# Kernel optimization log

Measured on AMD Instinct MI355X. Metric: run time of the kernel, lower is better.

Reference implementation:

```python
import jax, jax.numpy as jnp
import numpy as np

EXP = 1          # module init arg `exp`
NEG = -1e9       # masked_fill value


def setup_inputs() -> dict:
    key = jax.random.key(0)
    k1, k2 = jax.random.split(key)
    lhs = jax.random.normal(k1, (8, 1023, 768), dtype=jnp.float32)
    rhs = jax.random.normal(k2, (8, 8192, 768), dtype=jnp.float32)
    return {"lhs": lhs, "rhs": rhs}


def reference(lhs, rhs):
    # lhs: [B, N_1, dim], rhs: [B, N_, dim], N = N_1 + 1, F = N_ // N
    B, N1, d = lhs.shape
    N = N1 + 1
    Ntot = rhs.shape[1]
    F = Ntot // N

    # L2-normalize along feature dim (normalize_vector)
    ln = lhs / jnp.linalg.norm(lhs, axis=-1, keepdims=True)
    rn = rhs / jnp.linalg.norm(rhs, axis=-1, keepdims=True)

    # cosine similarity: [B, N_1, N_]
    sim = jnp.einsum('bnd,bmd->bnm', ln, rn) ** EXP

    # Diagonal-window mask on the [B, N_1, F, N] view:
    #  - column 0 of each N-block -> NEG
    #  - last N_1 columns (indices 1..N_1) -> NEG except where col-1 == row
    keep = jnp.concatenate(
        [jnp.zeros((N1, 1), dtype=bool), jnp.eye(N1, dtype=bool)], axis=-1
    )  # [N_1, N]
    sim4 = sim.reshape(B, N1, F, N)
    sim4 = jnp.where(keep[None, :, None, :], sim4, NEG)
    return sim4.reshape(B, N1, Ntot)
```

## Files before the change

### kernel.cpp

```cpp
#include <hip/hip_runtime.h>

constexpr int B    = 8;
constexpr int N1   = 1023;
constexpr int NBLK = 1024;
constexpr int D    = 768;
constexpr int F    = 8;
constexpr int NTOT = 8192;
constexpr float NEG = -1e9f;

typedef float v4f __attribute__((ext_vector_type(4)));

__global__ __launch_bounds__(256)
void lcs_kernel(const float* __restrict__ lhs,
                const float* __restrict__ rhs,
                float* __restrict__ out) {
    int t    = threadIdx.x;
    int wave = t >> 6;
    int lane = t & 63;

    int bid = blockIdx.x;
    int g   = bid / 9;
    int p   = bid - g * 9;

    v4f neg4 = {NEG, NEG, NEG, NEG};

    if (p == 0) {
        int row = g * 4 + wave;
        int n   = row % N1;
        int ol  = ((n + 1) >> 2) >> 3;

        v4f* o4 = (v4f*)out + (size_t)row * (NTOT / 4);
        #pragma unroll
        for (int it = 0; it < 32; ++it) {
            if (((it * 8 + (lane >> 3)) & 31) != ol) {
                __builtin_nontemporal_store(neg4, &o4[it * 64 + lane]);
            }
        }
    } else {
        int dot_id = g * 8 + (p - 1);
        int gi     = dot_id * 4 + wave;

        int n   = gi % N1;
        int tmp = gi / N1;
        int f   = tmp % F;
        int b   = tmp / F;

        const v4f* l4 = (const v4f*)(lhs + ((size_t)b * N1 + n) * D);
        const v4f* r4 = (const v4f*)(rhs + ((size_t)b * NTOT + (size_t)f * NBLK + (n + 1)) * D);

        v4f a0 = l4[lane];
        v4f a1 = l4[lane + 64];
        v4f a2 = l4[lane + 128];
        v4f c0 = __builtin_nontemporal_load(&r4[lane]);
        v4f c1 = __builtin_nontemporal_load(&r4[lane + 64]);
        v4f c2 = __builtin_nontemporal_load(&r4[lane + 128]);

        float dot = a0.x*c0.x + a0.y*c0.y + a0.z*c0.z + a0.w*c0.w
                  + a1.x*c1.x + a1.y*c1.y + a1.z*c1.z + a1.w*c1.w
                  + a2.x*c2.x + a2.y*c2.y + a2.z*c2.z + a2.w*c2.w;
        float l2  = a0.x*a0.x + a0.y*a0.y + a0.z*a0.z + a0.w*a0.w
                  + a1.x*a1.x + a1.y*a1.y + a1.z*a1.z + a1.w*a1.w
                  + a2.x*a2.x + a2.y*a2.y + a2.z*a2.z + a2.w*a2.w;
        float r2  = c0.x*c0.x + c0.y*c0.y + c0.z*c0.z + c0.w*c0.w
                  + c1.x*c1.x + c1.y*c1.y + c1.z*c1.z + c1.w*c1.w
                  + c2.x*c2.x + c2.y*c2.y + c2.z*c2.z + c2.w*c2.w;

        #pragma unroll
        for (int off = 32; off >= 1; off >>= 1) {
            dot += __shfl_xor(dot, off, 64);
            l2  += __shfl_xor(l2,  off, 64);
            r2  += __shfl_xor(r2,  off, 64);
        }
        float sim = dot * rsqrtf(l2 * r2);

        int keep_col = n + 1;
        int q_seg    = keep_col >> 2;
        int own_base = q_seg & ~7;
        if (lane < 8) {
            int qidx = own_base + lane;
            v4f v = neg4;
            if (qidx == q_seg) v[keep_col & 3] = sim;
            v4f* o4 = (v4f*)(out + ((size_t)b * N1 + n) * NTOT + (size_t)f * NBLK);
            __builtin_nontemporal_store(v, &o4[qidx]);
        }
    }
}

extern "C" void kernel_launch(void* const* d_in, const int* in_sizes, int n_in,
                              void* d_out, int out_size, void* d_ws, size_t ws_size,
                              hipStream_t stream) {
    const float* lhs = (const float*)d_in[0];
    const float* rhs = (const float*)d_in[1];
    float* out = (float*)d_out;

    int grid = 18414;
    lcs_kernel<<<grid, 256, 0, stream>>>(lhs, rhs, out);
}
```

Baseline: 84.24 us.

## Compute four F-blocks per wave to reuse lhs row and its norm

```diff
diff --git a/kernel.cpp b/kernel.cpp
--- a/kernel.cpp
+++ b/kernel.cpp
@@ -19,8 +19,8 @@
     int lane = t & 63;
 
     int bid = blockIdx.x;
-    int g   = bid / 9;
-    int p   = bid - g * 9;
+    int g   = bid / 3;
+    int p   = bid - g * 3;
 
     v4f neg4 = {NEG, NEG, NEG, NEG};
 
@@ -37,51 +37,63 @@
             }
         }
     } else {
-        int dot_id = g * 8 + (p - 1);
-        int gi     = dot_id * 4 + wave;
-
+        int gi  = (g * 2 + (p - 1)) * 4 + wave;
         int n   = gi % N1;
         int tmp = gi / N1;
-        int f   = tmp % F;
-        int b   = tmp / F;
+        int h   = tmp & 1;
+        int b   = tmp >> 1;
 
         const v4f* l4 = (const v4f*)(lhs + ((size_t)b * N1 + n) * D);
-        const v4f* r4 = (const v4f*)(rhs + ((size_t)b * NTOT + (size_t)f * NBLK + (n + 1)) * D);
-
         v4f a0 = l4[lane];
         v4f a1 = l4[lane + 64];
         v4f a2 = l4[lane + 128];
-        v4f c0 = __builtin_nontemporal_load(&r4[lane]);
-        v4f c1 = __builtin_nontemporal_load(&r4[lane + 64]);
-        v4f c2 = __builtin_nontemporal_load(&r4[lane + 128]);
 
-        float dot = a0.x*c0.x + a0.y*c0.y + a0.z*c0.z + a0.w*c0.w
-                  + a1.x*c1.x + a1.y*c1.y + a1.z*c1.z + a1.w*c1.w
-                  + a2.x*c2.x + a2.y*c2.y + a2.z*c2.z + a2.w*c2.w;
-        float l2  = a0.x*a0.x + a0.y*a0.y + a0.z*a0.z + a0.w*a0.w
-                  + a1.x*a1.x + a1.y*a1.y + a1.z*a1.z + a1.w*a1.w
-                  + a2.x*a2.x + a2.y*a2.y + a2.z*a2.z + a2.w*a2.w;
-        float r2  = c0.x*c0.x + c0.y*c0.y + c0.z*c0.z + c0.w*c0.w
-                  + c1.x*c1.x + c1.y*c1.y + c1.z*c1.z + c1.w*c1.w
-                  + c2.x*c2.x + c2.y*c2.y + c2.z*c2.z + c2.w*c2.w;
+        const v4f* rbase = (const v4f*)rhs
+            + ((size_t)b * NTOT + (size_t)h * 4 * NBLK + (n + 1)) * (D / 4);
+        constexpr size_t FSTR = (size_t)NBLK * (D / 4);
 
+        v4f c0[4], c1[4], c2[4];
         #pragma unroll
-        for (int off = 32; off >= 1; off >>= 1) {
-            dot += __shfl_xor(dot, off, 64);
-            l2  += __shfl_xor(l2,  off, 64);
-            r2  += __shfl_xor(r2,  off, 64);
+        for (int ff = 0; ff < 4; ++ff) {
+            const v4f* rf = rbase + (size_t)ff * FSTR;
+            c0[ff] = __builtin_nontemporal_load(rf + lane);
+            c1[ff] = __builtin_nontemporal_load(rf + lane + 64);
+            c2[ff] = __builtin_nontemporal_load(rf + lane + 128);
         }
-        float sim = dot * rsqrtf(l2 * r2);
+
+        float l2 = a0.x*a0.x + a0.y*a0.y + a0.z*a0.z + a0.w*a0.w
+                 + a1.x*a1.x + a1.y*a1.y + a1.z*a1.z + a1.w*a1.w
+                 + a2.x*a2.x + a2.y*a2.y + a2.z*a2.z + a2.w*a2.w;
+        #pragma unroll
+        for (int off = 32; off >= 1; off >>= 1) l2 += __shfl_xor(l2, off, 64);
 
         int keep_col = n + 1;
         int q_seg    = keep_col >> 2;
         int own_base = q_seg & ~7;
-        if (lane < 8) {
-            int qidx = own_base + lane;
-            v4f v = neg4;
-            if (qidx == q_seg) v[keep_col & 3] = sim;
-            v4f* o4 = (v4f*)(out + ((size_t)b * N1 + n) * NTOT + (size_t)f * NBLK);
-            __builtin_nontemporal_store(v, &o4[qidx]);
+        int r        = keep_col & 3;
+        v4f* orow = (v4f*)(out + ((size_t)b * N1 + n) * NTOT);
+
+        #pragma unroll
+        for (int ff = 0; ff < 4; ++ff) {
+            float dt = a0.x*c0[ff].x + a0.y*c0[ff].y + a0.z*c0[ff].z + a0.w*c0[ff].w
+                     + a1.x*c1[ff].x + a1.y*c1[ff].y + a1.z*c1[ff].z + a1.w*c1[ff].w
+                     + a2.x*c2[ff].x + a2.y*c2[ff].y + a2.z*c2[ff].z + a2.w*c2[ff].w;
+            float r2 = c0[ff].x*c0[ff].x + c0[ff].y*c0[ff].y + c0[ff].z*c0[ff].z + c0[ff].w*c0[ff].w
+                     + c1[ff].x*c1[ff].x + c1[ff].y*c1[ff].y + c1[ff].z*c1[ff].z + c1[ff].w*c1[ff].w
+                     + c2[ff].x*c2[ff].x + c2[ff].y*c2[ff].y + c2[ff].z*c2[ff].z + c2[ff].w*c2[ff].w;
+            #pragma unroll
+            for (int off = 32; off >= 1; off >>= 1) {
+                dt += __shfl_xor(dt, off, 64);
+                r2 += __shfl_xor(r2, off, 64);
+            }
+            float sim = dt * rsqrtf(l2 * r2);
+
+            if (lane < 8) {
+                int qidx = own_base + lane;
+                v4f v = neg4;
+                if (qidx == q_seg) v[r] = sim;
+                __builtin_nontemporal_store(v, &orow[(size_t)(h * 4 + ff) * 256 + qidx]);
+            }
         }
     }
 }
@@ -93,6 +105,6 @@
     const float* rhs = (const float*)d_in[1];
     float* out = (float*)d_out;
 
-    int grid = 18414;
+    int grid = 6138;
     lcs_kernel<<<grid, 256, 0, stream>>>(lhs, rhs, out);
 }
```

After: 83.99 us. About the same (-0.3%).
